# Kernel optimization log

Hardware: AMD Instinct MI355X
Metric: run time of the kernel (lower is better)

Reference implementation:

```python
import jax, jax.numpy as jnp
import numpy as np

H = 768   # encoder hidden size
NH = 4    # boundary attention heads
HD = H // NH
E = 9     # ent_type_size
R = 12    # rel_type_size
D = 64    # inner_dim
B = 4
S = 1024


def setup_inputs() -> dict:
    key = jax.random.key(0)
    ks = jax.random.split(key, 8)
    n = lambda k, shp: jax.random.normal(k, shp, jnp.float32) * 0.02
    return dict(
        hidden_states=jax.random.normal(ks[0], (B, S, H), jnp.float32),
        attention_mask=jnp.ones((B, S), jnp.float32),
        in_proj_w=n(ks[1], (3 * H, H)), in_proj_b=jnp.zeros((3 * H,), jnp.float32),
        out_proj_w=n(ks[2], (H, H)), out_proj_b=jnp.zeros((H,), jnp.float32),
        gate_w=n(ks[3], (H, H)), gate_b=jnp.zeros((H,), jnp.float32),
        ln_g=jnp.ones((H,), jnp.float32), ln_b=jnp.zeros((H,), jnp.float32),
        ent_w=n(ks[4], (E * 2 * D, H)), ent_b=jnp.zeros((E * 2 * D,), jnp.float32),
        prior_w=n(ks[5], (H, E)), prior_b=jnp.zeros((H,), jnp.float32),
        rel_w=n(ks[6], (R * 2 * D, 2 * H)), rel_b=jnp.zeros((R * 2 * D,), jnp.float32),
    )


def _sinusoidal_pos_emb(seq_len, dim, dtype):
    pos = jnp.arange(seq_len, dtype=dtype)[:, None]                 # [S,1]
    inv = jnp.power(jnp.asarray(10000.0, dtype), -2.0 * jnp.arange(dim // 2, dtype=dtype) / dim)
    ang = pos * inv                                                  # [S,D/2]
    emb = jnp.stack([jnp.sin(ang), jnp.cos(ang)], axis=-1).reshape(seq_len, dim)  # [sin0,cos0,sin1,cos1,...]
    return emb


def _gp_matrix(hs, W, b, mask):
    # hs: [B,S,Hin], W: [T*2D, Hin], mask: [B,S]
    bsz, seq_len, _ = hs.shape
    out = hs @ W.T + b                                               # [B,S,T*2D]
    T = out.shape[-1] // (2 * D)
    out = out.reshape(bsz, seq_len, T, 2 * D)
    qw, kw = out[..., :D], out[..., D:]                              # [B,S,T,D]
    # RoPE
    pe = _sinusoidal_pos_emb(seq_len, D, hs.dtype)                   # [S,D]
    cos = jnp.repeat(pe[:, 1::2], 2, axis=-1)[None, :, None, :]      # [1,S,1,D]
    sin = jnp.repeat(pe[:, ::2], 2, axis=-1)[None, :, None, :]

    def rot(x):
        x2 = jnp.stack([-x[..., 1::2], x[..., ::2]], axis=-1).reshape(x.shape)
        return x * cos + x2 * sin

    qw, kw = rot(qw), rot(kw)
    logits = jnp.einsum('bmtd,bntd->btmn', qw, kw)                   # [B,T,S,S]
    pad = mask[:, None, None, :]                                     # masks key dim
    logits = logits * pad - (1.0 - pad) * 1e12
    tril = jnp.tril(jnp.ones((seq_len, seq_len), logits.dtype), -1)
    logits = logits - tril * 1e12                                    # strictly lower triangle masked
    return logits / jnp.sqrt(jnp.asarray(D, logits.dtype))


def _boundary_attention(hs, mask, in_proj_w, in_proj_b, out_proj_w, out_proj_b,
                        gate_w, gate_b, ln_g, ln_b):
    bsz, seq_len, _ = hs.shape
    qkv = hs @ in_proj_w.T + in_proj_b                               # [B,S,3H]
    q, k, v = jnp.split(qkv, 3, axis=-1)
    q = q.reshape(bsz, seq_len, NH, HD)
    k = k.reshape(bsz, seq_len, NH, HD)
    v = v.reshape(bsz, seq_len, NH, HD)
    scores = jnp.einsum('bqhd,bkhd->bhqk', q, k) / jnp.sqrt(jnp.asarray(HD, hs.dtype))
    key_pad = (mask == 0)[:, None, None, :]                          # [B,1,1,S]
    scores = jnp.where(key_pad, jnp.asarray(-1e9, hs.dtype), scores)
    attn = jax.nn.softmax(scores, axis=-1)
    ctx = jnp.einsum('bhqk,bkhd->bqhd', attn, v).reshape(bsz, seq_len, H)
    attn_out = ctx @ out_proj_w.T + out_proj_b
    gate = jax.nn.sigmoid(attn_out @ gate_w.T + gate_b)
    x = hs + gate * attn_out
    mu = jnp.mean(x, axis=-1, keepdims=True)
    var = jnp.var(x, axis=-1, keepdims=True)
    return (x - mu) / jnp.sqrt(var + 1e-5) * ln_g + ln_b


def reference(hidden_states, attention_mask, in_proj_w, in_proj_b, out_proj_w, out_proj_b,
              gate_w, gate_b, ln_g, ln_b, ent_w, ent_b, prior_w, prior_b, rel_w, rel_b):
    enhanced = _boundary_attention(hidden_states, attention_mask, in_proj_w, in_proj_b,
                                   out_proj_w, out_proj_b, gate_w, gate_b, ln_g, ln_b)
    ent_logits = _gp_matrix(enhanced, ent_w, ent_b, attention_mask)  # [B,E,S,S]
    ent_prior = jnp.max(ent_logits, axis=-1)                          # [B,E,S]
    ent_prior = jnp.swapaxes(ent_prior, 1, 2)                         # [B,S,E]
    prior_feat = jax.nn.relu(ent_prior @ prior_w.T + prior_b)         # [B,S,H]
    rel_hidden = jnp.concatenate([enhanced, prior_feat], axis=-1)     # [B,S,2H]
    rel_logits = _gp_matrix(rel_hidden, rel_w, rel_b, attention_mask) # [B,R,S,S]
    return (ent_logits, rel_logits, enhanced)
```

## Files before the change

### kernel.cpp

```cpp
#include <hip/hip_runtime.h>
#include <math.h>

#define H_   768
#define NH_  4
#define HD_  192
#define E_   9
#define R_   12
#define D_   64
#define B_   4
#define S_   1024
#define H3_  (3 * H_)
#define MBS_ (B_ * S_)

typedef unsigned short u16;
typedef __attribute__((ext_vector_type(4))) int   i32x4;
typedef __attribute__((ext_vector_type(4))) float f32x4;

static const long OUT_REL_OFF = (long)B_ * E_ * S_ * S_;
static const long OUT_ENH_OFF = OUT_REL_OFF + (long)B_ * R_ * S_ * S_;

__device__ __forceinline__ u16 f2bf(float f) {
    unsigned u = __builtin_bit_cast(unsigned, f);
    return (u16)((u + 0x7fffu + ((u >> 16) & 1u)) >> 16);
}
__device__ __forceinline__ float bf2f(u16 h) {
    return __builtin_bit_cast(float, (unsigned)h << 16);
}
__device__ __forceinline__ void gload16(const u16* g, u16* l) {
    __builtin_amdgcn_global_load_lds(
        (__attribute__((address_space(1))) void*)g,
        (__attribute__((address_space(3))) void*)l, 16, 0, 0);
}
__device__ __forceinline__ void mfma_bf16(f32x4& acc, i32x4 a, i32x4 b) {
    asm volatile("v_mfma_f32_16x16x32_bf16 %0, %1, %2, %0"
                 : "+v"(acc) : "v"(a), "v"(b));
}

template<int BM, int BN, int EPI, int OBF, int PIPE>
__global__ __launch_bounds__(256) void gemm_mfma(
    const u16* __restrict__ A, const u16* __restrict__ Bw,
    const float* __restrict__ bias, void* __restrict__ Cv,
    int K, int lda, int ldb, int ldc, int nh,
    long sAb, long sAh, long sBb, long sBh, long sCb, long sCh,
    const float* __restrict__ mask, float scale, float* __restrict__ aux)
{
    constexpr int MI = BM / 32, NJ = BN / 32;
    constexpr int BUFE = (BM + BN) * 64;
    constexpr int LPS  = BM / 32 + BN / 32;
    const int z = blockIdx.z;
    const int zb = z / nh, zh = z - zb * nh;
    A  += zb * sAb + zh * sAh;
    Bw += zb * sBb + zh * sBh;

    const int gx = gridDim.x, gy = gridDim.y;
    int id = blockIdx.y * gx + blockIdx.x;
    const int nwg = gx * gy;
    if ((nwg & 7) == 0) id = (id & 7) * (nwg >> 3) + (id >> 3);
    const int bx = id % gx, by = id / gx;
    const int m0 = by * BM, n0 = bx * BN;

    __shared__ u16 lds[(PIPE ? 2 : 1) * BUFE];

    const int t = threadIdx.x;
    const int lane = t & 63, wid = t >> 6;
    const int wr = wid >> 1, wc = wid & 1;
    const int l16 = lane & 15, l4 = lane >> 4;

    auto stage = [&](int kt, u16* la) {
        u16* lb = la + BM * 64;
        const int k0 = kt << 6;
        #pragma unroll
        for (int i = 0; i < BM / 32; ++i) {
            const int e = i * 256 + t;
            const int row = e >> 3;
            const int c = ((e & 7) ^ (row & 7)) << 3;
            gload16(A + (long)(m0 + row) * lda + k0 + c, la + e * 8);
        }
        #pragma unroll
        for (int i = 0; i < BN / 32; ++i) {
            const int e = i * 256 + t;
            const int row = e >> 3;
            const int c = ((e & 7) ^ (row & 7)) << 3;
            gload16(Bw + (long)(n0 + row) * ldb + k0 + c, lb + e * 8);
        }
    };

    f32x4 acc[MI][NJ];
    #pragma unroll
    for (int mi = 0; mi < MI; ++mi)
        #pragma unroll
        for (int nj = 0; nj < NJ; ++nj)
            #pragma unroll
            for (int q = 0; q < 4; ++q) acc[mi][nj][q] = 0.0f;

    const int nt = K >> 6;

    if (PIPE == 0) {
        stage(0, lds);
        __syncthreads();
        const u16* la = lds;
        const u16* lb = lds + BM * 64;
        i32x4 af[MI][2], bfr[NJ][2];
        #pragma unroll
        for (int mi = 0; mi < MI; ++mi)
            #pragma unroll
            for (int kk = 0; kk < 2; ++kk) {
                const int row = wr * (BM / 2) + mi * 16 + l16;
                af[mi][kk] = *(const i32x4*)&la[row * 64 + ((((kk << 2) + l4) ^ (row & 7)) << 3)];
            }
        #pragma unroll
        for (int nj = 0; nj < NJ; ++nj)
            #pragma unroll
            for (int kk = 0; kk < 2; ++kk) {
                const int row = wc * (BN / 2) + nj * 16 + l16;
                bfr[nj][kk] = *(const i32x4*)&lb[row * 64 + ((((kk << 2) + l4) ^ (row & 7)) << 3)];
            }
        #pragma unroll
        for (int kk = 0; kk < 2; ++kk)
            #pragma unroll
            for (int mi = 0; mi < MI; ++mi)
                #pragma unroll
                for (int nj = 0; nj < NJ; ++nj)
                    mfma_bf16(acc[mi][nj], af[mi][kk], bfr[nj][kk]);
    } else {
        stage(0, lds);
        if (nt > 1) stage(1, lds + BUFE);
        for (int tt = 0; tt < nt; ++tt) {
            if (tt + 1 < nt) {
                if constexpr (LPS == 8) asm volatile("s_waitcnt vmcnt(8)" ::: "memory");
                else if constexpr (LPS == 7) asm volatile("s_waitcnt vmcnt(7)" ::: "memory");
                else if constexpr (LPS == 6) asm volatile("s_waitcnt vmcnt(6)" ::: "memory");
                else asm volatile("s_waitcnt vmcnt(5)" ::: "memory");
            } else {
                asm volatile("s_waitcnt vmcnt(0)" ::: "memory");
            }
            __builtin_amdgcn_s_barrier();
            u16* la = lds + (tt & 1) * BUFE;
            const u16* lb = la + BM * 64;
            i32x4 af[MI][2], bfr[NJ][2];
            #pragma unroll
            for (int mi = 0; mi < MI; ++mi)
                #pragma unroll
                for (int kk = 0; kk < 2; ++kk) {
                    const int row = wr * (BM / 2) + mi * 16 + l16;
                    af[mi][kk] = *(const i32x4*)&la[row * 64 + ((((kk << 2) + l4) ^ (row & 7)) << 3)];
                }
            #pragma unroll
            for (int nj = 0; nj < NJ; ++nj)
                #pragma unroll
                for (int kk = 0; kk < 2; ++kk) {
                    const int row = wc * (BN / 2) + nj * 16 + l16;
                    bfr[nj][kk] = *(const i32x4*)&lb[row * 64 + ((((kk << 2) + l4) ^ (row & 7)) << 3)];
                }
            asm volatile("s_waitcnt lgkmcnt(0)" ::: "memory");
            __builtin_amdgcn_sched_barrier(0);
            __builtin_amdgcn_s_barrier();
            if (tt + 2 < nt) stage(tt + 2, la);
            #pragma unroll
            for (int kk = 0; kk < 2; ++kk)
                #pragma unroll
                for (int mi = 0; mi < MI; ++mi)
                    #pragma unroll
                    for (int nj = 0; nj < NJ; ++nj)
                        mfma_bf16(acc[mi][nj], af[mi][kk], bfr[nj][kk]);
        }
        __syncthreads();
    }
    __builtin_amdgcn_sched_barrier(0);
    asm volatile("s_nop 7");
    asm volatile("s_nop 7");
    __builtin_amdgcn_sched_barrier(0);

    if (EPI == 1 || EPI == 3) mask += (long)zb * S_;
    const long cbase = zb * sCb + zh * sCh;

    float red[MI][4];
    if (EPI == 3) {
        #pragma unroll
        for (int mi = 0; mi < MI; ++mi)
            #pragma unroll
            for (int r = 0; r < 4; ++r) red[mi][r] = -INFINITY;
    }

    #pragma unroll
    for (int mi = 0; mi < MI; ++mi) {
        #pragma unroll
        for (int nj = 0; nj < NJ; ++nj) {
            const int gn = n0 + wc * (BN / 2) + nj * 16 + l16;
            const float bv = ((EPI == 0 || EPI == 4 || EPI == 7) && bias) ? bias[gn] : 0.0f;
            float invf = 0.0f;
            if (EPI == 4) invf = exp2f(-(float)((gn & 63) >> 1) * 0.41524101186092503f);
            #pragma unroll
            for (int r = 0; r < 4; ++r) {
                const int gm = m0 + wr * (BM / 2) + mi * 16 + l4 * 4 + r;
                float v = acc[mi][nj][r];
                const long cidx = cbase + (long)gm * ldc + gn;
                if (EPI == 0) {
                    v += bv;
                    if (OBF) ((u16*)Cv)[cidx] = f2bf(v);
                    else     ((float*)Cv)[cidx] = v;
                } else if (EPI == 7) {
                    v += bv;
                    const u16 bfv = f2bf(v);
                    ((u16*)Cv)[cidx] = bfv;
                    if (gn >= 2 * H_) {
                        const int hh = (gn - 2 * H_) / HD_;
                        const int dd = (gn - 2 * H_) - hh * HD_;
                        const int bb = gm >> 10, ss = gm & (S_ - 1);
                        ((u16*)aux)[((long)(bb * NH_ + hh) * HD_ + dd) * S_ + ss] = bfv;
                    }
                } else if (EPI == 1 || EPI == 3) {
                    const float pad = mask[gn];
                    v = v * pad - (1.0f - pad) * 1e12f;
                    if (gm > gn) v -= 1e12f;
                    v *= 0.125f;
                    ((float*)Cv)[cidx] = v;
                    if (EPI == 3) red[mi][r] = fmaxf(red[mi][r], v);
                } else {
                    v += bv;
                    const int sp = gm & (S_ - 1);
                    float sn, cs;
                    __sincosf((float)sp * invf, &sn, &cs);
                    const float pv = __shfl_xor(v, 1, 64);
                    v = (gn & 1) ? fmaf(v, cs, pv * sn) : fmaf(v, cs, -pv * sn);
                    ((u16*)Cv)[cidx] = f2bf(v);
                }
            }
        }
    }

    if (EPI == 3) {
        #pragma unroll
        for (int mi = 0; mi < MI; ++mi) {
            #pragma unroll
            for (int r = 0; r < 4; ++r) {
                float m = red[mi][r];
                m = fmaxf(m, __shfl_xor(m, 1, 64));
                m = fmaxf(m, __shfl_xor(m, 2, 64));
                m = fmaxf(m, __shfl_xor(m, 4, 64));
                m = fmaxf(m, __shfl_xor(m, 8, 64));
                if (l16 == 0) {
                    const int gm = m0 + wr * (BM / 2) + mi * 16 + l4 * 4 + r;
                    aux[((long)z * S_ + gm) * 16 + bx * 2 + wc] = m;
                }
            }
        }
    }
}

__global__ __launch_bounds__(256) void attn_fused(
    const u16* __restrict__ qkv, const u16* __restrict__ vt,
    const float* __restrict__ mask, u16* __restrict__ ctx, float qscale)
{
    const int z = blockIdx.y;
    const int b = z >> 2, h = z & 3;
    const int s0 = blockIdx.x * 32;
    const int t = threadIdx.x;
    const int lane = t & 63, w = t >> 6;
    const int l16 = lane & 15, l4 = lane >> 4;

    __shared__ u16 k_lds[64 * 192];
    __shared__ u16 v_lds[192 * 64];
    __shared__ u16 p_lds[32 * 64];
    __shared__ float rs_lds[4][32];

    i32x4 qf[2][6];
    {
        const u16* qb = qkv + (long)(b * S_ + s0 + l16) * H3_ + h * HD_;
        #pragma unroll
        for (int mi = 0; mi < 2; ++mi)
            #pragma unroll
            for (int kk = 0; kk < 6; ++kk)
                qf[mi][kk] = *(const i32x4*)(qb + (long)mi * 16 * H3_ + kk * 32 + l4 * 8);
    }
    asm volatile("s_waitcnt vmcnt(0)" ::: "memory");

    f32x4 acc_c[2][3];
    #pragma unroll
    for (int mi = 0; mi < 2; ++mi)
        #pragma unroll
        for (int nj = 0; nj < 3; ++nj)
            #pragma unroll
            for (int q = 0; q < 4; ++q) acc_c[mi][nj][q] = 0.0f;
    float rs_acc[2][4] = {};

    const float* mrow = mask + (long)b * S_;

    for (int kt = 0; kt < 16; ++kt) {
        const int kv0 = kt * 64;
        #pragma unroll
        for (int i = 0; i < 6; ++i) {
            const int e = i * 256 + t;
            const int row = e / 24;
            const int g = e - row * 24;
            const int gs = (g & ~7) | ((g & 7) ^ (row & 7));
            gload16(qkv + (long)(b * S_ + kv0 + row) * H3_ + H_ + h * HD_ + gs * 8,
                    k_lds + e * 8);
        }
        #pragma unroll
        for (int i = 0; i < 6; ++i) {
            const int e = i * 256 + t;
            const int row = e >> 3, g = e & 7;
            const int gs = g ^ (row & 7);
            gload16(vt + ((long)z * HD_ + row) * S_ + kv0 + gs * 8,
                    v_lds + e * 8);
        }
        asm volatile("s_waitcnt vmcnt(6)" ::: "memory");
        __builtin_amdgcn_s_barrier();

        f32x4 acc_s[2];
        #pragma unroll
        for (int mi = 0; mi < 2; ++mi)
            #pragma unroll
            for (int q = 0; q < 4; ++q) acc_s[mi][q] = 0.0f;
        #pragma unroll
        for (int kk = 0; kk < 6; ++kk) {
            const int krow = w * 16 + l16;
            const int g = kk * 4 + l4;
            const int gs = (g & ~7) | ((g & 7) ^ (krow & 7));
            const i32x4 kf = *(const i32x4*)&k_lds[krow * 192 + gs * 8];
            #pragma unroll
            for (int mi = 0; mi < 2; ++mi)
                mfma_bf16(acc_s[mi], qf[mi][kk], kf);
        }
        __builtin_amdgcn_sched_barrier(0);
        asm volatile("s_nop 7");
        asm volatile("s_nop 7");
        __builtin_amdgcn_sched_barrier(0);

        {
            const int coll = w * 16 + l16;
            const float mk = mrow[kv0 + coll];
            #pragma unroll
            for (int mi = 0; mi < 2; ++mi) {
                float rsp = 0.0f;
                #pragma unroll
                for (int r = 0; r < 4; ++r) {
                    const int rowl = mi * 16 + l4 * 4 + r;
                    float tv = 0.0f;
                    if (mk != 0.0f) tv = __expf(acc_s[mi][r] * qscale);
                    const int gs = (coll >> 3) ^ (rowl & 7);
                    p_lds[rowl * 64 + gs * 8 + (coll & 7)] = f2bf(tv);
                    rsp = tv;
                    float v = rsp;
                    v += __shfl_xor(v, 1, 64);
                    v += __shfl_xor(v, 2, 64);
                    v += __shfl_xor(v, 4, 64);
                    v += __shfl_xor(v, 8, 64);
                    rs_acc[mi][r] += v;
                }
            }
        }

        asm volatile("s_waitcnt vmcnt(0) lgkmcnt(0)" ::: "memory");
        __builtin_amdgcn_sched_barrier(0);
        __builtin_amdgcn_s_barrier();

        #pragma unroll
        for (int kk = 0; kk < 2; ++kk) {
            i32x4 pf[2];
            #pragma unroll
            for (int mi = 0; mi < 2; ++mi) {
                const int row = mi * 16 + l16;
                const int gs = (kk * 4 + l4) ^ (row & 7);
                pf[mi] = *(const i32x4*)&p_lds[row * 64 + gs * 8];
            }
            #pragma unroll
            for (int nj = 0; nj < 3; ++nj) {
                const int row = w * 48 + nj * 16 + l16;
                const int gs = (kk * 4 + l4) ^ (row & 7);
                const i32x4 vf = *(const i32x4*)&v_lds[row * 64 + gs * 8];
                #pragma unroll
                for (int mi = 0; mi < 2; ++mi)
                    mfma_bf16(acc_c[mi][nj], pf[mi], vf);
            }
        }
        __builtin_amdgcn_s_barrier();
    }

    __builtin_amdgcn_sched_barrier(0);
    asm volatile("s_nop 7");
    asm volatile("s_nop 7");
    __builtin_amdgcn_sched_barrier(0);

    if (l16 == 0) {
        #pragma unroll
        for (int mi = 0; mi < 2; ++mi)
            #pragma unroll
            for (int r = 0; r < 4; ++r)
                rs_lds[w][mi * 16 + l4 * 4 + r] = rs_acc[mi][r];
    }
    __syncthreads();

    #pragma unroll
    for (int mi = 0; mi < 2; ++mi) {
        #pragma unroll
        for (int r = 0; r < 4; ++r) {
            const int rowl = mi * 16 + l4 * 4 + r;
            const float inv = 1.0f / (rs_lds[0][rowl] + rs_lds[1][rowl] +
                                      rs_lds[2][rowl] + rs_lds[3][rowl]);
            #pragma unroll
            for (int nj = 0; nj < 3; ++nj) {
                const int d = w * 48 + nj * 16 + l16;
                ctx[(long)(b * S_ + s0 + rowl) * H_ + h * HD_ + d] =
                    f2bf(acc_c[mi][nj][r] * inv);
            }
        }
    }
}

__global__ __launch_bounds__(256) void cast_all(
    const float* __restrict__ hs, const float* __restrict__ ipw,
    const float* __restrict__ opw, const float* __restrict__ gw,
    const float* __restrict__ entw, const float* __restrict__ relw,
    const float* __restrict__ opb, const float* __restrict__ gb,
    u16* hs_o, u16* ipw_o, u16* opw_o, u16* gw_o, u16* entw_o, u16* relw_o,
    float* bias2)
{
    const int blk = blockIdx.x;
    if (blk >= 9120) {
        const float* src = (blk == 9120) ? opb : gb;
        float* dst = bias2 + (blk - 9120) * H_;
        if (threadIdx.x < 192)
            *(float4*)&dst[threadIdx.x * 4] = *(const float4*)&src[threadIdx.x * 4];
        return;
    }
    const float* in; u16* out; long base;
    if      (blk < 3072) { in = hs;   out = hs_o;   base = (long)blk * 1024; }
    else if (blk < 4800) { in = ipw;  out = ipw_o;  base = (long)(blk - 3072) * 1024; }
    else if (blk < 5376) { in = opw;  out = opw_o;  base = (long)(blk - 4800) * 1024; }
    else if (blk < 5952) { in = gw;   out = gw_o;   base = (long)(blk - 5376) * 1024; }
    else if (blk < 6816) { in = entw; out = entw_o; base = (long)(blk - 5952) * 1024; }
    else                 { in = relw; out = relw_o; base = (long)(blk - 6816) * 1024; }
    const long idx = base + (long)threadIdx.x * 4;
    const float4 v = *(const float4*)&in[idx];
    ushort4 o; o.x = f2bf(v.x); o.y = f2bf(v.y); o.z = f2bf(v.z); o.w = f2bf(v.w);
    *(ushort4*)&out[idx] = o;
}

__global__ __launch_bounds__(256) void gate_ln_bf(
    const float* __restrict__ hs, const u16* __restrict__ aogl,
    const float* __restrict__ g, const float* __restrict__ bta,
    float* __restrict__ enh, u16* __restrict__ relh)
{
    const long row = blockIdx.x;
    const float* hrow = hs + row * H_;
    const u16* arow = aogl + row * (2 * H_);
    const int tid = threadIdx.x;
    float x[3];
    float sum = 0.0f, sq = 0.0f;
    #pragma unroll
    for (int i = 0; i < 3; ++i) {
        const int j = tid + i * 256;
        const float a = bf2f(arow[j]);
        const float gt = 1.0f / (1.0f + __expf(-bf2f(arow[H_ + j])));
        const float xv = hrow[j] + gt * a;
        x[i] = xv; sum += xv; sq += xv * xv;
    }
    __shared__ float sm[8];
    #pragma unroll
    for (int o = 32; o > 0; o >>= 1) {
        sum += __shfl_xor(sum, o, 64);
        sq  += __shfl_xor(sq, o, 64);
    }
    const int lane = tid & 63, wid = tid >> 6;
    if (lane == 0) { sm[wid] = sum; sm[4 + wid] = sq; }
    __syncthreads();
    sum = sm[0] + sm[1] + sm[2] + sm[3];
    sq  = sm[4] + sm[5] + sm[6] + sm[7];
    const float mu = sum * (1.0f / (float)H_);
    float var = sq * (1.0f / (float)H_) - mu * mu;
    var = fmaxf(var, 0.0f);
    const float inv = 1.0f / sqrtf(var + 1e-5f);
    #pragma unroll
    for (int i = 0; i < 3; ++i) {
        const int j = tid + i * 256;
        const float o = (x[i] - mu) * inv * g[j] + bta[j];
        enh[row * H_ + j] = o;
        relh[row * (2 * H_) + j] = f2bf(o);
    }
}

__global__ __launch_bounds__(256) void prior_fused(
    const float* __restrict__ pmax, const float* __restrict__ pw,
    const float* __restrict__ pb, u16* __restrict__ relh)
{
    const int row = blockIdx.x;
    const int b = row >> 10, m = row & (S_ - 1);
    __shared__ float pr[E_];
    const int tid = threadIdx.x;
    if (tid < E_) {
        const float* pp = pmax + ((long)(b * E_ + tid) * S_ + m) * 16;
        float mx = -INFINITY;
        #pragma unroll
        for (int i = 0; i < 16; ++i) mx = fmaxf(mx, pp[i]);
        pr[tid] = mx;
    }
    __syncthreads();
    float p[E_];
    #pragma unroll
    for (int e = 0; e < E_; ++e) p[e] = pr[e];
    u16* orow = relh + (long)row * (2 * H_) + H_;
    #pragma unroll
    for (int i = 0; i < 3; ++i) {
        const int j = tid + i * 256;
        float a = pb[j];
        #pragma unroll
        for (int e = 0; e < E_; ++e) a = fmaf(p[e], pw[j * E_ + e], a);
        orow[j] = f2bf(fmaxf(a, 0.0f));
    }
}

extern "C" void kernel_launch(void* const* d_in, const int* in_sizes, int n_in,
                              void* d_out, int out_size, void* d_ws, size_t ws_size,
                              hipStream_t stream)
{
    const float* hs   = (const float*)d_in[0];
    const float* mask = (const float*)d_in[1];
    const float* ipw  = (const float*)d_in[2];
    const float* ipb  = (const float*)d_in[3];
    const float* opw  = (const float*)d_in[4];
    const float* opb  = (const float*)d_in[5];
    const float* gw   = (const float*)d_in[6];
    const float* gb   = (const float*)d_in[7];
    const float* lng  = (const float*)d_in[8];
    const float* lnb  = (const float*)d_in[9];
    const float* entw = (const float*)d_in[10];
    const float* entb = (const float*)d_in[11];
    const float* prw  = (const float*)d_in[12];
    const float* prb  = (const float*)d_in[13];
    const float* relw = (const float*)d_in[14];
    const float* relb = (const float*)d_in[15];
    float* out = (float*)d_out;
    char* base = (char*)d_ws;

    u16* ipw_bf  = (u16*)(base + 0);
    u16* opw_bf  = (u16*)(base + 3538944);
    u16* gw_bf   = (u16*)(base + 4718592);
    u16* entw_bf = (u16*)(base + 5898240);
    u16* relw_bf = (u16*)(base + 7667712);
    u16* hs_bf   = (u16*)(base + 12386304);
    u16* qkv_bf  = (u16*)(base + 18677760);
    u16* vt_bf   = (u16*)(base + 37552128);
    u16* ctx_bf  = (u16*)(base + 77398016);
    u16* aogl_bf = (u16*)(base + 83689472);
    float* bias2 = (float*)(base + 96272384);
    float* pmax  = (float*)(base + 97329152);
    u16* relh_bf = (u16*)(base + 43843584);
    u16* projr   = (u16*)(base + 56426496);
    float* enh   = out + OUT_ENH_OFF;

    const float qscale = 0.07216878364870323f;

    cast_all<<<9122, 256, 0, stream>>>(hs, ipw, opw, gw, entw, relw, opb, gb,
                                       hs_bf, ipw_bf, opw_bf, gw_bf, entw_bf, relw_bf,
                                       bias2);

    gemm_mfma<128,96,7,1,1><<<dim3(24, 32, 1), 256, 0, stream>>>(
        hs_bf, ipw_bf, ipb, qkv_bf, H_, H_, H_, H3_, 1,
        0,0,0,0,0,0, nullptr, 0.0f, (float*)vt_bf);

    attn_fused<<<dim3(32, 16), 256, 0, stream>>>(
        qkv_bf, vt_bf, mask, ctx_bf, qscale);

    gemm_mfma<128,96,0,1,1><<<dim3(16, 32, 1), 256, 0, stream>>>(
        ctx_bf, opw_bf, bias2, aogl_bf, H_, H_, H_, 2 * H_, 1,
        0,0,0,0,0,0, nullptr, 0.0f, nullptr);

    gate_ln_bf<<<MBS_, 256, 0, stream>>>(hs, aogl_bf, lng, lnb, enh, relh_bf);

    gemm_mfma<64,96,4,1,1><<<dim3(12, 64, 1), 256, 0, stream>>>(
        relh_bf, entw_bf, entb, projr, H_, 2 * H_, H_, E_ * 2 * D_, 1,
        0,0,0,0,0,0, nullptr, 0.0f, nullptr);

    gemm_mfma<128,128,3,0,0><<<dim3(8, 8, B_ * E_), 256, 0, stream>>>(
        projr, projr + D_, nullptr, out, D_, E_ * 2 * D_, E_ * 2 * D_, S_, E_,
        (long)S_ * E_ * 2 * D_, 2 * D_, (long)S_ * E_ * 2 * D_, 2 * D_,
        (long)E_ * S_ * S_, (long)S_ * S_, mask, 0.0f, pmax);

    prior_fused<<<MBS_, 256, 0, stream>>>(pmax, prw, prb, relh_bf);

    gemm_mfma<128,96,4,1,1><<<dim3(16, 32, 1), 256, 0, stream>>>(
        relh_bf, relw_bf, relb, projr, 2 * H_, 2 * H_, 2 * H_, R_ * 2 * D_, 1,
        0,0,0,0,0,0, nullptr, 0.0f, nullptr);

    gemm_mfma<128,128,1,0,0><<<dim3(8, 8, B_ * R_), 256, 0, stream>>>(
        projr, projr + D_, nullptr, out + OUT_REL_OFF, D_, R_ * 2 * D_, R_ * 2 * D_, S_, R_,
        (long)S_ * R_ * 2 * D_, 2 * D_, (long)S_ * R_ * 2 * D_, 2 * D_,
        (long)R_ * S_ * S_, (long)S_ * S_, mask, 0.0f, nullptr);

    (void)in_sizes; (void)n_in; (void)out_size; (void)ws_size;
}
```

Baseline: 246.9 us.

## Stage masked logits through LDS for coalesced stores, add setprio, tweak pipeline

For the masked-logits epilogues (EPI 1/3), results are written into padded LDS in four row chunks and then stored with coalesced float4 global writes, replacing scattered per-lane scalar stores. The non-pipelined GEMM path now loops over all K tiles instead of handling only one, and the QKV GEMM switches to that non-pipelined path. The attention kernel raises wave priority around its MFMA sections. The LDS staging adds barriers per chunk and hardcodes a 128-wide tile layout (wc*64, wr*64) for these epilogues.

```diff
diff --git a/kernel.cpp b/kernel.cpp
--- a/kernel.cpp
+++ b/kernel.cpp
@@ -96,32 +96,35 @@
     const int nt = K >> 6;
 
     if (PIPE == 0) {
-        stage(0, lds);
-        __syncthreads();
-        const u16* la = lds;
-        const u16* lb = lds + BM * 64;
-        i32x4 af[MI][2], bfr[NJ][2];
-        #pragma unroll
-        for (int mi = 0; mi < MI; ++mi)
-            #pragma unroll
-            for (int kk = 0; kk < 2; ++kk) {
-                const int row = wr * (BM / 2) + mi * 16 + l16;
-                af[mi][kk] = *(const i32x4*)&la[row * 64 + ((((kk << 2) + l4) ^ (row & 7)) << 3)];
-            }
-        #pragma unroll
-        for (int nj = 0; nj < NJ; ++nj)
-            #pragma unroll
-            for (int kk = 0; kk < 2; ++kk) {
-                const int row = wc * (BN / 2) + nj * 16 + l16;
-                bfr[nj][kk] = *(const i32x4*)&lb[row * 64 + ((((kk << 2) + l4) ^ (row & 7)) << 3)];
-            }
-        #pragma unroll
-        for (int kk = 0; kk < 2; ++kk)
+        for (int tt = 0; tt < nt; ++tt) {
+            stage(tt, lds);
+            __syncthreads();
+            const u16* la = lds;
+            const u16* lb = lds + BM * 64;
+            i32x4 af[MI][2], bfr[NJ][2];
             #pragma unroll
             for (int mi = 0; mi < MI; ++mi)
                 #pragma unroll
-                for (int nj = 0; nj < NJ; ++nj)
-                    mfma_bf16(acc[mi][nj], af[mi][kk], bfr[nj][kk]);
+                for (int kk = 0; kk < 2; ++kk) {
+                    const int row = wr * (BM / 2) + mi * 16 + l16;
+                    af[mi][kk] = *(const i32x4*)&la[row * 64 + ((((kk << 2) + l4) ^ (row & 7)) << 3)];
+                }
+            #pragma unroll
+            for (int nj = 0; nj < NJ; ++nj)
+                #pragma unroll
+                for (int kk = 0; kk < 2; ++kk) {
+                    const int row = wc * (BN / 2) + nj * 16 + l16;
+                    bfr[nj][kk] = *(const i32x4*)&lb[row * 64 + ((((kk << 2) + l4) ^ (row & 7)) << 3)];
+                }
+            #pragma unroll
+            for (int kk = 0; kk < 2; ++kk)
+                #pragma unroll
+                for (int mi = 0; mi < MI; ++mi)
+                    #pragma unroll
+                    for (int nj = 0; nj < NJ; ++nj)
+                        mfma_bf16(acc[mi][nj], af[mi][kk], bfr[nj][kk]);
+            __syncthreads();
+        }
     } else {
         stage(0, lds);
         if (nt > 1) stage(1, lds + BUFE);
@@ -174,74 +177,105 @@
     if (EPI == 1 || EPI == 3) mask += (long)zb * S_;
     const long cbase = zb * sCb + zh * sCh;
 
-    float red[MI][4];
-    if (EPI == 3) {
-        #pragma unroll
-        for (int mi = 0; mi < MI; ++mi)
-            #pragma unroll
-            for (int r = 0; r < 4; ++r) red[mi][r] = -INFINITY;
-    }
-
-    #pragma unroll
-    for (int mi = 0; mi < MI; ++mi) {
-        #pragma unroll
-        for (int nj = 0; nj < NJ; ++nj) {
-            const int gn = n0 + wc * (BN / 2) + nj * 16 + l16;
-            const float bv = ((EPI == 0 || EPI == 4 || EPI == 7) && bias) ? bias[gn] : 0.0f;
-            float invf = 0.0f;
-            if (EPI == 4) invf = exp2f(-(float)((gn & 63) >> 1) * 0.41524101186092503f);
-            #pragma unroll
-            for (int r = 0; r < 4; ++r) {
-                const int gm = m0 + wr * (BM / 2) + mi * 16 + l4 * 4 + r;
-                float v = acc[mi][nj][r];
-                const long cidx = cbase + (long)gm * ldc + gn;
-                if (EPI == 0) {
-                    v += bv;
-                    if (OBF) ((u16*)Cv)[cidx] = f2bf(v);
-                    else     ((float*)Cv)[cidx] = v;
-                } else if (EPI == 7) {
-                    v += bv;
-                    const u16 bfv = f2bf(v);
-                    ((u16*)Cv)[cidx] = bfv;
-                    if (gn >= 2 * H_) {
-                        const int hh = (gn - 2 * H_) / HD_;
-                        const int dd = (gn - 2 * H_) - hh * HD_;
-                        const int bb = gm >> 10, ss = gm & (S_ - 1);
-                        ((u16*)aux)[((long)(bb * NH_ + hh) * HD_ + dd) * S_ + ss] = bfv;
+    if constexpr (EPI == 1 || EPI == 3) {
+        float red[MI][4];
+        if (EPI == 3) {
+            #pragma unroll
+            for (int mi = 0; mi < MI; ++mi)
+                #pragma unroll
+                for (int r = 0; r < 4; ++r) red[mi][r] = -INFINITY;
+        }
+        float* tl = (float*)lds;
+        constexpr int LDP = 132;
+        #pragma unroll
+        for (int c = 0; c < 4; ++c) {
+            __syncthreads();
+            if (wr == (c >> 1)) {
+                #pragma unroll
+                for (int mih = 0; mih < 2; ++mih) {
+                    const int mi = (c & 1) * 2 + mih;
+                    #pragma unroll
+                    for (int nj = 0; nj < NJ; ++nj) {
+                        const int gnl = wc * 64 + nj * 16 + l16;
+                        const int gn = n0 + gnl;
+                        const float pad = mask[gn];
+                        #pragma unroll
+                        for (int r = 0; r < 4; ++r) {
+                            const int gm = m0 + wr * 64 + mi * 16 + l4 * 4 + r;
+                            float v = acc[mi][nj][r];
+                            v = v * pad - (1.0f - pad) * 1e12f;
+                            if (gm > gn) v -= 1e12f;
+                            v *= 0.125f;
+                            if (EPI == 3) red[mi][r] = fmaxf(red[mi][r], v);
+                            tl[(mih * 16 + l4 * 4 + r) * LDP + gnl] = v;
+                        }
                     }
-                } else if (EPI == 1 || EPI == 3) {
-                    const float pad = mask[gn];
-                    v = v * pad - (1.0f - pad) * 1e12f;
-                    if (gm > gn) v -= 1e12f;
-                    v *= 0.125f;
-                    ((float*)Cv)[cidx] = v;
-                    if (EPI == 3) red[mi][r] = fmaxf(red[mi][r], v);
-                } else {
-                    v += bv;
-                    const int sp = gm & (S_ - 1);
-                    float sn, cs;
-                    __sincosf((float)sp * invf, &sn, &cs);
-                    const float pv = __shfl_xor(v, 1, 64);
-                    v = (gn & 1) ? fmaf(v, cs, pv * sn) : fmaf(v, cs, -pv * sn);
-                    ((u16*)Cv)[cidx] = f2bf(v);
-                }
-            }
-        }
-    }
-
-    if (EPI == 3) {
+                }
+            }
+            __syncthreads();
+            #pragma unroll
+            for (int j = 0; j < 4; ++j) {
+                const int idx = j * 256 + t;
+                const int rowl = idx >> 5, f4 = idx & 31;
+                const float4 vv = *(const float4*)&tl[rowl * LDP + f4 * 4];
+                const int gm = m0 + c * 32 + rowl;
+                *(float4*)&((float*)Cv)[cbase + (long)gm * ldc + n0 + f4 * 4] = vv;
+            }
+        }
+        if (EPI == 3) {
+            #pragma unroll
+            for (int mi = 0; mi < MI; ++mi) {
+                #pragma unroll
+                for (int r = 0; r < 4; ++r) {
+                    float m = red[mi][r];
+                    m = fmaxf(m, __shfl_xor(m, 1, 64));
+                    m = fmaxf(m, __shfl_xor(m, 2, 64));
+                    m = fmaxf(m, __shfl_xor(m, 4, 64));
+                    m = fmaxf(m, __shfl_xor(m, 8, 64));
+                    if (l16 == 0) {
+                        const int gm = m0 + wr * (BM / 2) + mi * 16 + l4 * 4 + r;
+                        aux[((long)z * S_ + gm) * 16 + bx * 2 + wc] = m;
+                    }
+                }
+            }
+        }
+    } else {
         #pragma unroll
         for (int mi = 0; mi < MI; ++mi) {
             #pragma unroll
-            for (int r = 0; r < 4; ++r) {
-                float m = red[mi][r];
-                m = fmaxf(m, __shfl_xor(m, 1, 64));
-                m = fmaxf(m, __shfl_xor(m, 2, 64));
-                m = fmaxf(m, __shfl_xor(m, 4, 64));
-                m = fmaxf(m, __shfl_xor(m, 8, 64));
-                if (l16 == 0) {
+            for (int nj = 0; nj < NJ; ++nj) {
+                const int gn = n0 + wc * (BN / 2) + nj * 16 + l16;
+                const float bv = (bias != nullptr) ? bias[gn] : 0.0f;
+                float invf = 0.0f;
+                if (EPI == 4) invf = exp2f(-(float)((gn & 63) >> 1) * 0.41524101186092503f);
+                #pragma unroll
+                for (int r = 0; r < 4; ++r) {
                     const int gm = m0 + wr * (BM / 2) + mi * 16 + l4 * 4 + r;
-                    aux[((long)z * S_ + gm) * 16 + bx * 2 + wc] = m;
+                    float v = acc[mi][nj][r];
+                    const long cidx = cbase + (long)gm * ldc + gn;
+                    if (EPI == 0) {
+                        v += bv;
+                        if (OBF) ((u16*)Cv)[cidx] = f2bf(v);
+                        else     ((float*)Cv)[cidx] = v;
+                    } else if (EPI == 7) {
+                        v += bv;
+                        const u16 bfv = f2bf(v);
+                        ((u16*)Cv)[cidx] = bfv;
+                        if (gn >= 2 * H_) {
+                            const int hh = (gn - 2 * H_) / HD_;
+                            const int dd = (gn - 2 * H_) - hh * HD_;
+                            const int bb = gm >> 10, ss = gm & (S_ - 1);
+                            ((u16*)aux)[((long)(bb * NH_ + hh) * HD_ + dd) * S_ + ss] = bfv;
+                        }
+                    } else {
+                        v += bv;
+                        const int sp = gm & (S_ - 1);
+                        float sn, cs;
+                        __sincosf((float)sp * invf, &sn, &cs);
+                        const float pv = __shfl_xor(v, 1, 64);
+                        v = (gn & 1) ? fmaf(v, cs, pv * sn) : fmaf(v, cs, -pv * sn);
+                        ((u16*)Cv)[cidx] = f2bf(v);
+                    }
                 }
             }
         }
@@ -313,6 +347,7 @@
         for (int mi = 0; mi < 2; ++mi)
             #pragma unroll
             for (int q = 0; q < 4; ++q) acc_s[mi][q] = 0.0f;
+        __builtin_amdgcn_s_setprio(1);
         #pragma unroll
         for (int kk = 0; kk < 6; ++kk) {
             const int krow = w * 16 + l16;
@@ -323,6 +358,7 @@
             for (int mi = 0; mi < 2; ++mi)
                 mfma_bf16(acc_s[mi], qf[mi][kk], kf);
         }
+        __builtin_amdgcn_s_setprio(0);
         __builtin_amdgcn_sched_barrier(0);
         asm volatile("s_nop 7");
         asm volatile("s_nop 7");
@@ -333,7 +369,6 @@
             const float mk = mrow[kv0 + coll];
             #pragma unroll
             for (int mi = 0; mi < 2; ++mi) {
-                float rsp = 0.0f;
                 #pragma unroll
                 for (int r = 0; r < 4; ++r) {
                     const int rowl = mi * 16 + l4 * 4 + r;
@@ -341,8 +376,7 @@
                     if (mk != 0.0f) tv = __expf(acc_s[mi][r] * qscale);
                     const int gs = (coll >> 3) ^ (rowl & 7);
                     p_lds[rowl * 64 + gs * 8 + (coll & 7)] = f2bf(tv);
-                    rsp = tv;
-                    float v = rsp;
+                    float v = tv;
                     v += __shfl_xor(v, 1, 64);
                     v += __shfl_xor(v, 2, 64);
                     v += __shfl_xor(v, 4, 64);
@@ -356,6 +390,7 @@
         __builtin_amdgcn_sched_barrier(0);
         __builtin_amdgcn_s_barrier();
 
+        __builtin_amdgcn_s_setprio(1);
         #pragma unroll
         for (int kk = 0; kk < 2; ++kk) {
             i32x4 pf[2];
@@ -375,6 +410,7 @@
                     mfma_bf16(acc_c[mi][nj], pf[mi], vf);
             }
         }
+        __builtin_amdgcn_s_setprio(0);
         __builtin_amdgcn_s_barrier();
     }
 
@@ -556,7 +592,7 @@
                                        hs_bf, ipw_bf, opw_bf, gw_bf, entw_bf, relw_bf,
                                        bias2);
 
-    gemm_mfma<128,96,7,1,1><<<dim3(24, 32, 1), 256, 0, stream>>>(
+    gemm_mfma<128,96,7,1,0><<<dim3(24, 32, 1), 256, 0, stream>>>(
         hs_bf, ipw_bf, ipb, qkv_bf, H_, H_, H_, H3_, 1,
         0,0,0,0,0,0, nullptr, 0.0f, (float*)vt_bf);
 
```

Result: no change. 245.5 us (-0.6%).
